# Optimization experiments

Measured on AMD Instinct MI355X. Metric: run time of the kernel, lower is better.

## Reference

```python
import jax, jax.numpy as jnp
import numpy as np

N, E = 50000, 800000
F_IN, H, C = 128, 8, 32  # hidden=256, heads=8 -> C=32
DROP_P = 0.6


def setup_inputs() -> dict:
    key = jax.random.key(0)
    ks = jax.random.split(key, 8)
    x = jax.random.normal(ks[0], (N, F_IN), dtype=jnp.float32)
    edge_index = jax.random.randint(ks[1], (2, E), 0, N, dtype=jnp.int64)
    # precomputed inverted-dropout masks (Bernoulli keep * 1/(1-p)), as passed via dp_mask args
    dp_mask = (jax.random.uniform(ks[2], (E, H)) > DROP_P).astype(jnp.float32) / (1.0 - DROP_P)
    dp_mask_self = (jax.random.uniform(ks[3], (N, H)) > DROP_P).astype(jnp.float32) / (1.0 - DROP_P)
    # learned parameters of GATConv
    W = jax.random.normal(ks[4], (F_IN, H * C), dtype=jnp.float32) * (1.0 / np.sqrt(F_IN))
    att_src = jax.random.normal(ks[5], (H, C), dtype=jnp.float32) * 0.1
    att_dst = jax.random.normal(ks[6], (H, C), dtype=jnp.float32) * 0.1
    bias = jnp.zeros((H * C,), dtype=jnp.float32)
    return {"x": x, "edge_index": edge_index, "dp_mask": dp_mask,
            "dp_mask_self": dp_mask_self, "W": W, "att_src": att_src,
            "att_dst": att_dst, "bias": bias}


def reference(x, edge_index, dp_mask, dp_mask_self, W, att_src, att_dst, bias):
    n = x.shape[0]
    h = (x @ W).reshape(n, H, C)                      # [N,H,C]
    a_src = jnp.sum(h * att_src, axis=-1)             # [N,H] source-side score
    a_dst = jnp.sum(h * att_dst, axis=-1)             # [N,H] dest-side score
    # flow='target_to_source': aggregate at edge_index[0], gather from edge_index[1]
    dst = edge_index[0]
    src = edge_index[1]
    e_alpha = jax.nn.leaky_relu(a_src[src] + a_dst[dst], 0.2)   # [E,H]
    s_alpha = jax.nn.leaky_relu(a_src + a_dst, 0.2)             # [N,H] self-loops
    seg = jnp.concatenate([dst, jnp.arange(n, dtype=dst.dtype)])
    alpha = jnp.concatenate([e_alpha, s_alpha], axis=0)         # [E+N,H]
    # segment softmax over each destination's neighborhood (incl. self-loop)
    m = jax.ops.segment_max(alpha, seg, num_segments=n)
    ex = jnp.exp(alpha - m[seg])
    denom = jax.ops.segment_sum(ex, seg, num_segments=n)
    p = ex / denom[seg]                                         # [E+N,H]
    # dropout on attention coefficients (masks passed in)
    p = p * jnp.concatenate([dp_mask, dp_mask_self], axis=0)
    msgs = jnp.concatenate([h[src], h], axis=0)                 # [E+N,H,C]
    out = jax.ops.segment_sum(p[:, :, None] * msgs, seg, num_segments=n)
    return out.reshape(n, H * C) + bias                         # concat heads + bias
```

## Files before the change

kernel.cpp:

```cpp
#include <hip/hip_runtime.h>

#define NN 50000
#define FIN 128
#define HC 256
#define NH 8
#define NE 800000
#define WROW 136
#define GEMMB 391
#define NBLK1 3516
#define OVFCAP 131072

typedef __attribute__((ext_vector_type(8))) short short8;
typedef __attribute__((ext_vector_type(4))) short short4v;
typedef __attribute__((ext_vector_type(4))) float floatx4;

__device__ __forceinline__ float bf2f(unsigned short u) {
    union { unsigned int i; float f; } v; v.i = ((unsigned int)u) << 16; return v.f;
}
__device__ __forceinline__ unsigned short f2bf(float f) {
    union { float f; unsigned int i; } v; v.f = f;
    unsigned int r = v.i + 0x7fffu + ((v.i >> 16) & 1u);
    return (unsigned short)(r >> 16);
}
__device__ __forceinline__ float lrelu(float x) { return x > 0.f ? x : 0.2f * x; }
__device__ __forceinline__ float ldf(const void* p, int f32, long long i) {
    return f32 ? ((const float*)p)[i] : bf2f(((const unsigned short*)p)[i]);
}
__device__ __forceinline__ int lde(const int* ei, int i64, long long i) {
    return i64 ? (int)((const long long*)ei)[i] : ei[i];
}
__device__ __forceinline__ float sel8(const float s[2][4], int t2, int rr) {
    float a0 = t2 ? s[1][0] : s[0][0];
    float a1 = t2 ? s[1][1] : s[0][1];
    float a2 = t2 ? s[1][2] : s[0][2];
    float a3 = t2 ? s[1][3] : s[0][3];
    return (rr == 0) ? a0 : ((rr == 1) ? a1 : ((rr == 2) ? a2 : a3));
}
__device__ __forceinline__ float blo(unsigned int u) {
    union { unsigned int i; float f; } v; v.i = u << 16; return v.f;
}
__device__ __forceinline__ float bhi(unsigned int u) {
    union { unsigned int i; float f; } v; v.i = u & 0xFFFF0000u; return v.f;
}
__device__ __forceinline__ float bperm(int addr, float v) {
    return __uint_as_float((unsigned int)__builtin_amdgcn_ds_bpermute(addr, (int)__float_as_uint(v)));
}

__global__ __launch_bounds__(256) void k_front(
        const void* __restrict__ x, const int* __restrict__ ei,
        const void* __restrict__ dpm, const void* __restrict__ W,
        const void* __restrict__ as_, const void* __restrict__ ad_,
        int* __restrict__ flags, unsigned short* __restrict__ h,
        float* __restrict__ a_src, float* __restrict__ a_dst,
        int* __restrict__ cnt, int* __restrict__ ovfcnt,
        unsigned int* __restrict__ bucket, int2* __restrict__ ovf,
        int cap, int capl2) {
    __shared__ unsigned short lwt[128 * WROW];
    __shared__ int s_bad, s_nz;
    const int tid = threadIdx.x;
    const int b = blockIdx.x;

    if (tid == 0) { s_bad = 0; s_nz = 0; }
    __syncthreads();
    {
        unsigned int wv = ((const unsigned int*)dpm)[tid];
        if (wv != 0u && wv != 0x40200000u) atomicAdd(&s_bad, 1);
        if (((const unsigned int*)ei)[2 * tid + 1] != 0u) atomicAdd(&s_nz, 1);
    }
    __syncthreads();
    const int f32 = (s_bad == 0) ? 1 : 0;
    const int i64 = (s_nz == 0) ? 1 : 0;
    if (b == 0 && tid == 0) { flags[0] = f32; flags[1] = i64; }

    if (b < GEMMB) {
        const int lane = tid & 63;
        const int wave = tid >> 6;
        const int lrow = lane & 15;
        const int quad = lane >> 4;
        const int row0w = b * 128 + wave * 32;

        short8 a[2][4];
        #pragma unroll
        for (int t = 0; t < 2; t++)
            #pragma unroll
            for (int q = 0; q < 4; q++)
                #pragma unroll
                for (int j = 0; j < 8; j++) a[t][q][j] = 0;

        #pragma unroll
        for (int t = 0; t < 2; t++) {
            int row = row0w + t * 16 + lrow;
            if (row < NN) {
                if (f32) {
                    const float* xp = (const float*)x + (long long)row * FIN + quad * 8;
                    #pragma unroll
                    for (int q = 0; q < 4; q++) {
                        floatx4 u0 = *(const floatx4*)(xp + q * 32);
                        floatx4 u1 = *(const floatx4*)(xp + q * 32 + 4);
                        #pragma unroll
                        for (int j = 0; j < 4; j++) {
                            a[t][q][j]     = (short)f2bf(u0[j]);
                            a[t][q][j + 4] = (short)f2bf(u1[j]);
                        }
                    }
                } else {
                    const unsigned short* xp = (const unsigned short*)x + (long long)row * FIN + quad * 8;
                    #pragma unroll
                    for (int q = 0; q < 4; q++) a[t][q] = *(const short8*)(xp + q * 32);
                }
            }
        }

        #pragma unroll
        for (int ch = 0; ch < 2; ch++) {
            if (ch) __syncthreads();
            {
                const int lcol = tid & 127;
                const int col = ch * 128 + lcol;
                const int k0 = (tid >> 7) * 64;
                if (f32) {
                    const float* wp = (const float*)W + col;
                    for (int k = k0; k < k0 + 64; k++) lwt[lcol * WROW + k] = f2bf(wp[(long long)k * HC]);
                } else {
                    const unsigned short* wp = (const unsigned short*)W + col;
                    for (int k = k0; k < k0 + 64; k++) lwt[lcol * WROW + k] = wp[(long long)k * HC];
                }
            }
            __syncthreads();

            float sS[2][4], sD[2][4];
            #pragma unroll 4
            for (int ct = 0; ct < 8; ct++) {
                if ((ct & 1) == 0) {
                    #pragma unroll
                    for (int t = 0; t < 2; t++)
                        #pragma unroll
                        for (int r = 0; r < 4; r++) { sS[t][r] = 0.f; sD[t][r] = 0.f; }
                }
                floatx4 acc0 = {0.f, 0.f, 0.f, 0.f};
                floatx4 acc1 = {0.f, 0.f, 0.f, 0.f};
                const unsigned short* wp = lwt + (ct * 16 + lrow) * WROW + quad * 8;
                #pragma unroll
                for (int q = 0; q < 4; q++) {
                    short8 bb = *(const short8*)(wp + q * 32);
                    acc0 = __builtin_amdgcn_mfma_f32_16x16x32_bf16(a[0][q], bb, acc0, 0, 0, 0);
                    acc1 = __builtin_amdgcn_mfma_f32_16x16x32_bf16(a[1][q], bb, acc1, 0, 0, 0);
                }
                const int gcol = ch * 128 + ct * 16 + lrow;
                #pragma unroll
                for (int r = 0; r < 4; r++) {
                    int orow = row0w + quad * 4 + r;
                    if (orow < NN) h[(long long)orow * HC + gcol] = f2bf(acc0[r]);
                    int orow1 = orow + 16;
                    if (orow1 < NN) h[(long long)orow1 * HC + gcol] = f2bf(acc1[r]);
                }
                float tS = ldf(as_, f32, gcol);
                float tD = ldf(ad_, f32, gcol);
                #pragma unroll
                for (int r = 0; r < 4; r++) {
                    sS[0][r] += acc0[r] * tS;  sS[1][r] += acc1[r] * tS;
                    sD[0][r] += acc0[r] * tD;  sD[1][r] += acc1[r] * tD;
                }
                if (ct & 1) {
                    #pragma unroll
                    for (int m = 1; m <= 8; m <<= 1)
                        #pragma unroll
                        for (int t = 0; t < 2; t++)
                            #pragma unroll
                            for (int r = 0; r < 4; r++) {
                                sS[t][r] += __shfl_xor(sS[t][r], m);
                                sD[t][r] += __shfl_xor(sD[t][r], m);
                            }
                    int hd = ch * 4 + (ct >> 1);
                    if (lrow < 8) {
                        int t2 = lrow >> 2, rr = lrow & 3;
                        int row = row0w + t2 * 16 + quad * 4 + rr;
                        if (row < NN) a_src[row * NH + hd] = sel8(sS, t2, rr);
                    } else {
                        int lr = lrow - 8;
                        int t2 = lr >> 2, rr = lr & 3;
                        int row = row0w + t2 * 16 + quad * 4 + rr;
                        if (row < NN) a_dst[row * NH + hd] = sel8(sD, t2, rr);
                    }
                }
            }
        }
    } else {
        const long long e = (long long)(b - GEMMB) * 256 + tid;
        int dst = lde(ei, i64, e);
        int src = lde(ei, i64, (long long)NE + e);
        unsigned int msk = 0;
        if (f32) {
            const floatx4* dp = (const floatx4*)((const float*)dpm + e * 8);
            floatx4 d0 = dp[0], d1 = dp[1];
            #pragma unroll
            for (int j = 0; j < 4; j++) {
                msk |= (d0[j] != 0.f ? 1u : 0u) << j;
                msk |= (d1[j] != 0.f ? 1u : 0u) << (4 + j);
            }
        } else {
            short8 dd = *(const short8*)((const unsigned short*)dpm + e * 8);
            #pragma unroll
            for (int j = 0; j < 8; j++) msk |= (dd[j] != 0 ? 1u : 0u) << j;
        }
        unsigned int entry = (unsigned int)src | (msk << 16);
        int pos = atomicAdd(&cnt[dst], 1);
        if (pos < cap) bucket[((long long)dst << capl2) + pos] = entry;
        else {
            int op = atomicAdd(ovfcnt, 1);
            if (op < OVFCAP) ovf[op] = make_int2(dst, (int)entry);
        }
    }
}

__global__ __launch_bounds__(256) void k_aggr(
        const int* __restrict__ cnt, const int* __restrict__ ovfcnt,
        const unsigned int* __restrict__ bucket, const int2* __restrict__ ovf,
        const float* __restrict__ a_src, const float* __restrict__ a_dst,
        const unsigned short* __restrict__ h, const void* __restrict__ dps,
        const int* __restrict__ flags, const void* __restrict__ bs_,
        void* __restrict__ out, int cap, int capl2) {
    const int wid = blockIdx.x * 4 + (threadIdx.x >> 6);
    const int lane = threadIdx.x & 63;
    const int nA = wid * 2;
    if (nA >= NN) return;
    const int uA = __builtin_amdgcn_readfirstlane(nA);
    const int uB = uA + 1;
    const int f32 = flags[0];
    int novf = *ovfcnt; novf = novf > OVFCAP ? OVFCAP : novf;
    int mnA = cnt[uA]; mnA = mnA < cap ? mnA : cap;
    int mnB = cnt[uB]; mnB = mnB < cap ? mnB : cap;
    const unsigned int* __restrict__ bpA = bucket + ((long long)uA << capl2);
    const unsigned int* __restrict__ bpB = bucket + ((long long)uB << capl2);

    const int hh = lane >> 3;
    const int e8 = lane & 7;
    const int badr = (lane & 56) << 2;
    const int cb = lane * 4;
    const float adA = a_dst[uA * NH + hh];
    const float adB = a_dst[uB * NH + hh];

    float dnA = 0.f, dnB = 0.f;
    float aA0 = 0.f, aA1 = 0.f, aA2 = 0.f, aA3 = 0.f;
    float aB0 = 0.f, aB1 = 0.f, aB2 = 0.f, aB3 = 0.f;

    const int mx = mnA > mnB ? mnA : mnB;
    for (int j = 0; j < mx; j += 8) {
        unsigned int A0 = bpA[j + 0], A1 = bpA[j + 1], A2 = bpA[j + 2], A3 = bpA[j + 3],
                     A4 = bpA[j + 4], A5 = bpA[j + 5], A6 = bpA[j + 6], A7 = bpA[j + 7];
        unsigned int B0 = bpB[j + 0], B1 = bpB[j + 1], B2 = bpB[j + 2], B3 = bpB[j + 3],
                     B4 = bpB[j + 4], B5 = bpB[j + 5], B6 = bpB[j + 6], B7 = bpB[j + 7];

        const int idx = j + e8;
        int icA = idx < mnA ? idx : (mnA > 0 ? mnA - 1 : 0);
        int icB = idx < mnB ? idx : (mnB > 0 ? mnB - 1 : 0);
        unsigned int ueA = bpA[icA];
        unsigned int ueB = bpB[icB];
        float alA = a_src[(int)(ueA & 0xFFFFu) * NH + hh] + adA;
        float alB = a_src[(int)(ueB & 0xFFFFu) * NH + hh] + adB;
        float wA = __expf(fmaxf(alA, 0.2f * alA)); wA = idx < mnA ? wA : 0.f;
        float wB = __expf(fmaxf(alB, 0.2f * alB)); wB = idx < mnB ? wB : 0.f;
        dnA += wA; dnB += wB;
        float wsA = ((ueA >> (16 + hh)) & 1u) ? wA : -wA;
        float wsB = ((ueB >> (16 + hh)) & 1u) ? wB : -wB;

        #define GATW(N, K) float w##N##K = bperm(badr + 4 * K, ws##N);
        GATW(A,0) GATW(A,1) GATW(A,2) GATW(A,3) GATW(A,4) GATW(A,5) GATW(A,6) GATW(A,7)
        GATW(B,0) GATW(B,1) GATW(B,2) GATW(B,3) GATW(B,4) GATW(B,5) GATW(B,6) GATW(B,7)
        #undef GATW

        #define GATH(N, K) \
            const unsigned short* hp##N##K = h + \
                (((long long)(__builtin_amdgcn_readfirstlane((int)N##K) & 0xFFFF)) << 8); \
            uint2 v##N##K = make_uint2(0u, 0u); \
            if (w##N##K > 0.f) v##N##K = *(const uint2*)(hp##N##K + cb);
        GATH(A,0) GATH(A,1) GATH(A,2) GATH(A,3) GATH(A,4) GATH(A,5) GATH(A,6) GATH(A,7)
        GATH(B,0) GATH(B,1) GATH(B,2) GATH(B,3) GATH(B,4) GATH(B,5) GATH(B,6) GATH(B,7)
        #undef GATH

        #define MACC(N, K) { float p = w##N##K * 2.5f; \
            a##N##0 = fmaf(p, blo(v##N##K.x), a##N##0); a##N##1 = fmaf(p, bhi(v##N##K.x), a##N##1); \
            a##N##2 = fmaf(p, blo(v##N##K.y), a##N##2); a##N##3 = fmaf(p, bhi(v##N##K.y), a##N##3); }
        MACC(A,0) MACC(A,1) MACC(A,2) MACC(A,3) MACC(A,4) MACC(A,5) MACC(A,6) MACC(A,7)
        MACC(B,0) MACC(B,1) MACC(B,2) MACC(B,3) MACC(B,4) MACC(B,5) MACC(B,6) MACC(B,7)
        #undef MACC
    }

    dnA += __shfl_xor(dnA, 1); dnA += __shfl_xor(dnA, 2); dnA += __shfl_xor(dnA, 4);
    dnB += __shfl_xor(dnB, 1); dnB += __shfl_xor(dnB, 2); dnB += __shfl_xor(dnB, 4);

    for (int i = 0; i < novf; i++) {
        int2 tv = ovf[i];
        if (tv.x == nA || tv.x == uB) {
            unsigned int u = (unsigned int)tv.y;
            int src = (int)(u & 0xFFFFu);
            float ad = (tv.x == nA) ? adA : adB;
            float w = __expf(lrelu(a_src[src * NH + hh] + ad));
            uint2 hv = make_uint2(0u, 0u);
            if ((u >> (16 + hh)) & 1u) hv = *(const uint2*)(h + ((long long)src << 8) + cb);
            float p = w * 2.5f;
            if (tv.x == nA) {
                dnA += w;
                aA0 = fmaf(p, blo(hv.x), aA0); aA1 = fmaf(p, bhi(hv.x), aA1);
                aA2 = fmaf(p, blo(hv.y), aA2); aA3 = fmaf(p, bhi(hv.y), aA3);
            } else {
                dnB += w;
                aB0 = fmaf(p, blo(hv.x), aB0); aB1 = fmaf(p, bhi(hv.x), aB1);
                aB2 = fmaf(p, blo(hv.y), aB2); aB3 = fmaf(p, bhi(hv.y), aB3);
            }
        }
    }
    {
        float wSA = __expf(lrelu(a_src[uA * NH + hh] + adA));
        float wSB = __expf(lrelu(a_src[uB * NH + hh] + adB));
        dnA += wSA; dnB += wSB;
        float pSA = wSA * ldf(dps, f32, (long long)uA * NH + hh);
        float pSB = wSB * ldf(dps, f32, (long long)uB * NH + hh);
        uint2 hvA = *(const uint2*)(h + ((long long)uA << 8) + cb);
        uint2 hvB = *(const uint2*)(h + ((long long)uB << 8) + cb);
        aA0 = fmaf(pSA, blo(hvA.x), aA0); aA1 = fmaf(pSA, bhi(hvA.x), aA1);
        aA2 = fmaf(pSA, blo(hvA.y), aA2); aA3 = fmaf(pSA, bhi(hvA.y), aA3);
        aB0 = fmaf(pSB, blo(hvB.x), aB0); aB1 = fmaf(pSB, bhi(hvB.x), aB1);
        aB2 = fmaf(pSB, blo(hvB.y), aB2); aB3 = fmaf(pSB, bhi(hvB.y), aB3);
    }
    float invA = 1.0f / dnA, invB = 1.0f / dnB;
    float b0 = ldf(bs_, f32, cb + 0), b1 = ldf(bs_, f32, cb + 1);
    float b2 = ldf(bs_, f32, cb + 2), b3 = ldf(bs_, f32, cb + 3);
    if (f32) {
        floatx4 oA = {aA0 * invA + b0, aA1 * invA + b1, aA2 * invA + b2, aA3 * invA + b3};
        floatx4 oB = {aB0 * invB + b0, aB1 * invB + b1, aB2 * invB + b2, aB3 * invB + b3};
        *(floatx4*)((float*)out + (long long)uA * HC + cb) = oA;
        *(floatx4*)((float*)out + (long long)uB * HC + cb) = oB;
    } else {
        short4v oA, oB;
        oA[0] = (short)f2bf(aA0 * invA + b0); oA[1] = (short)f2bf(aA1 * invA + b1);
        oA[2] = (short)f2bf(aA2 * invA + b2); oA[3] = (short)f2bf(aA3 * invA + b3);
        oB[0] = (short)f2bf(aB0 * invB + b0); oB[1] = (short)f2bf(aB1 * invB + b1);
        oB[2] = (short)f2bf(aB2 * invB + b2); oB[3] = (short)f2bf(aB3 * invB + b3);
        *(short4v*)((unsigned short*)out + (long long)uA * HC + cb) = oA;
        *(short4v*)((unsigned short*)out + (long long)uB * HC + cb) = oB;
    }
}

extern "C" void kernel_launch(void* const* d_in, const int* in_sizes, int n_in,
                              void* d_out, int out_size, void* d_ws, size_t ws_size,
                              hipStream_t stream) {
    const void* x       = d_in[0];
    const int*  ei      = (const int*)d_in[1];
    const void* dp_mask = d_in[2];
    const void* dp_self = d_in[3];
    const void* W       = d_in[4];
    const void* att_s   = d_in[5];
    const void* att_d   = d_in[6];
    const void* bias    = d_in[7];

    char* w = (char*)d_ws;
    unsigned short* h      = (unsigned short*)(w + 0);
    float*          a_src  = (float*)(w + 25600000);
    float*          a_dst  = (float*)(w + 27200000);
    int*            cnt    = (int*)(w + 28800000);
    int*            ovfcnt = (int*)(w + 29000000);
    int*            flags  = (int*)(w + 29000064);
    int2*           ovf    = (int2*)(w + 29000960);
    unsigned int*   bucket = (unsigned int*)(w + 30049536);

    long long avail = (long long)ws_size - 30049536LL - 512LL;
    int cap = 64, capl2 = 6;
    while (cap > 4 && (long long)cap * 200000LL > avail) { cap >>= 1; capl2--; }

    hipMemsetAsync(cnt, 0, 200960, stream);
    k_front<<<NBLK1, 256, 0, stream>>>(x, ei, dp_mask, W, att_s, att_d,
                                       flags, h, a_src, a_dst, cnt, ovfcnt, bucket, ovf,
                                       cap, capl2);
    k_aggr<<<NN / 8, 256, 0, stream>>>(cnt, ovfcnt, bucket, ovf, a_src, a_dst, h,
                                       dp_self, flags, bias, d_out, cap, capl2);
}
```

Before: 209.4 us.

## Precompute per-edge attention weights into LDS and use nontemporal loads in bucketing

The aggregation kernel now computes all edge attention weights for both destination nodes up front, one edge per lane across all 8 heads. It loads a_src as vectorized float4 rows, stores signed weights in shared memory, and reads neighbor indices with readlane instead of per-iteration bucket loads and bpermutes. It also splits the front kernel's edge loads and stores into nontemporal accesses and moves the atomic earlier to overlap with mask decoding. This is meant to cut redundant bucket and a_src loads and cross-lane shuffles in the hot loop. In exchange it adds an LDS allocation and fixes the unrolled consume loop at 64 edges per node, so larger degrees rely on the cap and overflow path.

Result: faster. 201.1 us (median of 2 runs) (-4.0%).

```diff
diff --git a/kernel.cpp b/kernel.cpp
--- a/kernel.cpp
+++ b/kernel.cpp
@@ -26,9 +26,6 @@
 __device__ __forceinline__ float ldf(const void* p, int f32, long long i) {
     return f32 ? ((const float*)p)[i] : bf2f(((const unsigned short*)p)[i]);
 }
-__device__ __forceinline__ int lde(const int* ei, int i64, long long i) {
-    return i64 ? (int)((const long long*)ei)[i] : ei[i];
-}
 __device__ __forceinline__ float sel8(const float s[2][4], int t2, int rr) {
     float a0 = t2 ? s[1][0] : s[0][0];
     float a1 = t2 ? s[1][1] : s[0][1];
@@ -41,9 +38,6 @@
 }
 __device__ __forceinline__ float bhi(unsigned int u) {
     union { unsigned int i; float f; } v; v.i = u & 0xFFFF0000u; return v.f;
-}
-__device__ __forceinline__ float bperm(int addr, float v) {
-    return __uint_as_float((unsigned int)__builtin_amdgcn_ds_bpermute(addr, (int)__float_as_uint(v)));
 }
 
 __global__ __launch_bounds__(256) void k_front(
@@ -187,26 +181,41 @@
         }
     } else {
         const long long e = (long long)(b - GEMMB) * 256 + tid;
-        int dst = lde(ei, i64, e);
-        int src = lde(ei, i64, (long long)NE + e);
+        int dst, src;
+        if (i64) {
+            dst = (int)__builtin_nontemporal_load((const long long*)ei + e);
+            src = (int)__builtin_nontemporal_load((const long long*)ei + NE + e);
+        } else {
+            dst = __builtin_nontemporal_load(ei + e);
+            src = __builtin_nontemporal_load(ei + NE + e);
+        }
+        int pos;
         unsigned int msk = 0;
         if (f32) {
             const floatx4* dp = (const floatx4*)((const float*)dpm + e * 8);
-            floatx4 d0 = dp[0], d1 = dp[1];
+            floatx4 d0 = __builtin_nontemporal_load(dp);
+            floatx4 d1 = __builtin_nontemporal_load(dp + 1);
+            pos = atomicAdd(&cnt[dst], 1);
             #pragma unroll
             for (int j = 0; j < 4; j++) {
                 msk |= (d0[j] != 0.f ? 1u : 0u) << j;
                 msk |= (d1[j] != 0.f ? 1u : 0u) << (4 + j);
             }
         } else {
-            short8 dd = *(const short8*)((const unsigned short*)dpm + e * 8);
+            const short4v* dp = (const short4v*)((const unsigned short*)dpm + e * 8);
+            short4v d0 = __builtin_nontemporal_load(dp);
+            short4v d1 = __builtin_nontemporal_load(dp + 1);
+            pos = atomicAdd(&cnt[dst], 1);
             #pragma unroll
-            for (int j = 0; j < 8; j++) msk |= (dd[j] != 0 ? 1u : 0u) << j;
+            for (int j = 0; j < 4; j++) {
+                msk |= (d0[j] != 0 ? 1u : 0u) << j;
+                msk |= (d1[j] != 0 ? 1u : 0u) << (4 + j);
+            }
         }
         unsigned int entry = (unsigned int)src | (msk << 16);
-        int pos = atomicAdd(&cnt[dst], 1);
-        if (pos < cap) bucket[((long long)dst << capl2) + pos] = entry;
-        else {
+        if (pos < cap) {
+            __builtin_nontemporal_store(entry, &bucket[((long long)dst << capl2) + pos]);
+        } else {
             int op = atomicAdd(ovfcnt, 1);
             if (op < OVFCAP) ovf[op] = make_int2(dst, (int)entry);
         }
@@ -220,12 +229,14 @@
         const unsigned short* __restrict__ h, const void* __restrict__ dps,
         const int* __restrict__ flags, const void* __restrict__ bs_,
         void* __restrict__ out, int cap, int capl2) {
+    __shared__ float wsh[4 * 2 * 8 * 68];
     const int wid = blockIdx.x * 4 + (threadIdx.x >> 6);
     const int lane = threadIdx.x & 63;
     const int nA = wid * 2;
     if (nA >= NN) return;
     const int uA = __builtin_amdgcn_readfirstlane(nA);
     const int uB = uA + 1;
+    const int wave = threadIdx.x >> 6;
     const int f32 = flags[0];
     int novf = *ovfcnt; novf = novf > OVFCAP ? OVFCAP : novf;
     int mnA = cnt[uA]; mnA = mnA < cap ? mnA : cap;
@@ -233,73 +244,103 @@
     const unsigned int* __restrict__ bpA = bucket + ((long long)uA << capl2);
     const unsigned int* __restrict__ bpB = bucket + ((long long)uB << capl2);
 
+    const int half = lane >> 5;
+    const int l32 = lane & 31;
     const int hh = lane >> 3;
-    const int e8 = lane & 7;
-    const int badr = (lane & 56) << 2;
     const int cb = lane * 4;
-    const float adA = a_dst[uA * NH + hh];
-    const float adB = a_dst[uB * NH + hh];
+
+    const int mnH = half ? mnB : mnA;
+    const int unH = half ? uB : uA;
+    const unsigned int* __restrict__ bpH = half ? bpB : bpA;
+    float* __restrict__ wl = wsh + wave * (2 * 8 * 68) + half * (8 * 68);
+
+    int lc = l32 < mnH ? l32 : (mnH > 0 ? mnH - 1 : 0);
+    unsigned int ue = bpH[lc];
+    {
+        int esrc = (int)(ue & 0xFFFFu);
+        floatx4 as0 = *(const floatx4*)(a_src + esrc * NH);
+        floatx4 as1 = *(const floatx4*)(a_src + esrc * NH + 4);
+        floatx4 ad0 = *(const floatx4*)(a_dst + unH * NH);
+        floatx4 ad1 = *(const floatx4*)(a_dst + unH * NH + 4);
+        const bool valid = l32 < mnH;
+        #pragma unroll
+        for (int k = 0; k < 8; k++) {
+            float al = (k < 4 ? as0[k & 3] : as1[k & 3]) + (k < 4 ? ad0[k & 3] : ad1[k & 3]);
+            float w = __expf(fmaxf(al, 0.2f * al));
+            w = valid ? w : 0.f;
+            wl[k * 68 + l32] = ((ue >> (16 + k)) & 1u) ? w : -w;
+        }
+    }
+    unsigned int ue2 = 0u;
+    if (mnA > 32 || mnB > 32) {
+        int idx2 = 32 + l32;
+        int lc2 = idx2 < mnH ? idx2 : (mnH > 0 ? mnH - 1 : 0);
+        ue2 = bpH[lc2];
+        int esrc = (int)(ue2 & 0xFFFFu);
+        floatx4 as0 = *(const floatx4*)(a_src + esrc * NH);
+        floatx4 as1 = *(const floatx4*)(a_src + esrc * NH + 4);
+        floatx4 ad0 = *(const floatx4*)(a_dst + unH * NH);
+        floatx4 ad1 = *(const floatx4*)(a_dst + unH * NH + 4);
+        const bool valid = idx2 < mnH;
+        #pragma unroll
+        for (int k = 0; k < 8; k++) {
+            float al = (k < 4 ? as0[k & 3] : as1[k & 3]) + (k < 4 ? ad0[k & 3] : ad1[k & 3]);
+            float w = __expf(fmaxf(al, 0.2f * al));
+            w = valid ? w : 0.f;
+            wl[k * 68 + 32 + l32] = ((ue2 >> (16 + k)) & 1u) ? w : -w;
+        }
+    }
+    __asm__ volatile("s_waitcnt lgkmcnt(0)" ::: "memory");
 
     float dnA = 0.f, dnB = 0.f;
     float aA0 = 0.f, aA1 = 0.f, aA2 = 0.f, aA3 = 0.f;
     float aB0 = 0.f, aB1 = 0.f, aB2 = 0.f, aB3 = 0.f;
-
-    const int mx = mnA > mnB ? mnA : mnB;
-    for (int j = 0; j < mx; j += 8) {
-        unsigned int A0 = bpA[j + 0], A1 = bpA[j + 1], A2 = bpA[j + 2], A3 = bpA[j + 3],
-                     A4 = bpA[j + 4], A5 = bpA[j + 5], A6 = bpA[j + 6], A7 = bpA[j + 7];
-        unsigned int B0 = bpB[j + 0], B1 = bpB[j + 1], B2 = bpB[j + 2], B3 = bpB[j + 3],
-                     B4 = bpB[j + 4], B5 = bpB[j + 5], B6 = bpB[j + 6], B7 = bpB[j + 7];
-
-        const int idx = j + e8;
-        int icA = idx < mnA ? idx : (mnA > 0 ? mnA - 1 : 0);
-        int icB = idx < mnB ? idx : (mnB > 0 ? mnB - 1 : 0);
-        unsigned int ueA = bpA[icA];
-        unsigned int ueB = bpB[icB];
-        float alA = a_src[(int)(ueA & 0xFFFFu) * NH + hh] + adA;
-        float alB = a_src[(int)(ueB & 0xFFFFu) * NH + hh] + adB;
-        float wA = __expf(fmaxf(alA, 0.2f * alA)); wA = idx < mnA ? wA : 0.f;
-        float wB = __expf(fmaxf(alB, 0.2f * alB)); wB = idx < mnB ? wB : 0.f;
-        dnA += wA; dnB += wB;
-        float wsA = ((ueA >> (16 + hh)) & 1u) ? wA : -wA;
-        float wsB = ((ueB >> (16 + hh)) & 1u) ? wB : -wB;
-
-        #define GATW(N, K) float w##N##K = bperm(badr + 4 * K, ws##N);
-        GATW(A,0) GATW(A,1) GATW(A,2) GATW(A,3) GATW(A,4) GATW(A,5) GATW(A,6) GATW(A,7)
-        GATW(B,0) GATW(B,1) GATW(B,2) GATW(B,3) GATW(B,4) GATW(B,5) GATW(B,6) GATW(B,7)
-        #undef GATW
-
-        #define GATH(N, K) \
-            const unsigned short* hp##N##K = h + \
-                (((long long)(__builtin_amdgcn_readfirstlane((int)N##K) & 0xFFFF)) << 8); \
-            uint2 v##N##K = make_uint2(0u, 0u); \
-            if (w##N##K > 0.f) v##N##K = *(const uint2*)(hp##N##K + cb);
-        GATH(A,0) GATH(A,1) GATH(A,2) GATH(A,3) GATH(A,4) GATH(A,5) GATH(A,6) GATH(A,7)
-        GATH(B,0) GATH(B,1) GATH(B,2) GATH(B,3) GATH(B,4) GATH(B,5) GATH(B,6) GATH(B,7)
-        #undef GATH
-
-        #define MACC(N, K) { float p = w##N##K * 2.5f; \
-            a##N##0 = fmaf(p, blo(v##N##K.x), a##N##0); a##N##1 = fmaf(p, bhi(v##N##K.x), a##N##1); \
-            a##N##2 = fmaf(p, blo(v##N##K.y), a##N##2); a##N##3 = fmaf(p, bhi(v##N##K.y), a##N##3); }
-        MACC(A,0) MACC(A,1) MACC(A,2) MACC(A,3) MACC(A,4) MACC(A,5) MACC(A,6) MACC(A,7)
-        MACC(B,0) MACC(B,1) MACC(B,2) MACC(B,3) MACC(B,4) MACC(B,5) MACC(B,6) MACC(B,7)
-        #undef MACC
-    }
-
-    dnA += __shfl_xor(dnA, 1); dnA += __shfl_xor(dnA, 2); dnA += __shfl_xor(dnA, 4);
-    dnB += __shfl_xor(dnB, 1); dnB += __shfl_xor(dnB, 2); dnB += __shfl_xor(dnB, 4);
+    const float* __restrict__ wrA = wsh + wave * (2 * 8 * 68) + hh * 68;
+    const float* __restrict__ wrB = wrA + 8 * 68;
+
+    #pragma unroll
+    for (int c = 0; c < 8; c++) {
+        if (8 * c < mnA) {
+            #define CONSA(K) { \
+                float wv = wrA[8 * c + K]; \
+                dnA += fabsf(wv); \
+                int s = (c < 4 ? __builtin_amdgcn_readlane((int)ue, 8 * c + K) \
+                               : __builtin_amdgcn_readlane((int)ue2, 8 * c + K - 32)) & 0xFFFF; \
+                uint2 v = make_uint2(0u, 0u); \
+                if (wv > 0.f) v = *(const uint2*)(h + ((long long)s << 8) + cb); \
+                float p = wv * 2.5f; \
+                aA0 = fmaf(p, blo(v.x), aA0); aA1 = fmaf(p, bhi(v.x), aA1); \
+                aA2 = fmaf(p, blo(v.y), aA2); aA3 = fmaf(p, bhi(v.y), aA3); }
+            CONSA(0) CONSA(1) CONSA(2) CONSA(3) CONSA(4) CONSA(5) CONSA(6) CONSA(7)
+            #undef CONSA
+        }
+        if (8 * c < mnB) {
+            #define CONSB(K) { \
+                float wv = wrB[8 * c + K]; \
+                dnB += fabsf(wv); \
+                int s = (c < 4 ? __builtin_amdgcn_readlane((int)ue, 32 + 8 * c + K) \
+                               : __builtin_amdgcn_readlane((int)ue2, 8 * c + K)) & 0xFFFF; \
+                uint2 v = make_uint2(0u, 0u); \
+                if (wv > 0.f) v = *(const uint2*)(h + ((long long)s << 8) + cb); \
+                float p = wv * 2.5f; \
+                aB0 = fmaf(p, blo(v.x), aB0); aB1 = fmaf(p, bhi(v.x), aB1); \
+                aB2 = fmaf(p, blo(v.y), aB2); aB3 = fmaf(p, bhi(v.y), aB3); }
+            CONSB(0) CONSB(1) CONSB(2) CONSB(3) CONSB(4) CONSB(5) CONSB(6) CONSB(7)
+            #undef CONSB
+        }
+    }
 
     for (int i = 0; i < novf; i++) {
         int2 tv = ovf[i];
-        if (tv.x == nA || tv.x == uB) {
+        if (tv.x == uA || tv.x == uB) {
             unsigned int u = (unsigned int)tv.y;
             int src = (int)(u & 0xFFFFu);
-            float ad = (tv.x == nA) ? adA : adB;
-            float w = __expf(lrelu(a_src[src * NH + hh] + ad));
+            float adh = a_dst[tv.x * NH + hh];
+            float w = __expf(lrelu(a_src[src * NH + hh] + adh));
             uint2 hv = make_uint2(0u, 0u);
             if ((u >> (16 + hh)) & 1u) hv = *(const uint2*)(h + ((long long)src << 8) + cb);
             float p = w * 2.5f;
-            if (tv.x == nA) {
+            if (tv.x == uA) {
                 dnA += w;
                 aA0 = fmaf(p, blo(hv.x), aA0); aA1 = fmaf(p, bhi(hv.x), aA1);
                 aA2 = fmaf(p, blo(hv.y), aA2); aA3 = fmaf(p, bhi(hv.y), aA3);
@@ -311,8 +352,9 @@
         }
     }
     {
-        float wSA = __expf(lrelu(a_src[uA * NH + hh] + adA));
-        float wSB = __expf(lrelu(a_src[uB * NH + hh] + adB));
+        float adhA = a_dst[uA * NH + hh], adhB = a_dst[uB * NH + hh];
+        float wSA = __expf(lrelu(a_src[uA * NH + hh] + adhA));
+        float wSB = __expf(lrelu(a_src[uB * NH + hh] + adhB));
         dnA += wSA; dnB += wSB;
         float pSA = wSA * ldf(dps, f32, (long long)uA * NH + hh);
         float pSB = wSB * ldf(dps, f32, (long long)uB * NH + hh);
```
